# Performance work log

Hardware: AMD Instinct MI355X
Metric: run time of the kernel (lower is better)

## Reference

```python
import jax, jax.numpy as jnp
import numpy as np

B, S, D, DA, DP = 32, 4096, 256, 128, 64


def setup_inputs() -> dict:
    key = jax.random.key(0)
    ks = jax.random.split(key, 10)
    scale = 0.05
    return {
        "h": jax.random.normal(ks[0], (B, S, D), jnp.float32),
        "q": jax.random.normal(ks[1], (B, D), jnp.float32),
        "pf1": jax.random.normal(ks[2], (B, S, DP), jnp.float32),
        "pf2": jax.random.normal(ks[3], (B, S, DP), jnp.float32),
        "Wh": jax.random.normal(ks[4], (DA, D), jnp.float32) * scale,
        "Wq": jax.random.normal(ks[5], (DA, D), jnp.float32) * scale,
        "Wp1": jax.random.normal(ks[6], (DP, DP), jnp.float32) * scale,
        "Wp2": jax.random.normal(ks[7], (DP, DP), jnp.float32) * scale,
        "Wc": jax.random.normal(ks[8], (1, 2 * DA + 2 * DP), jnp.float32) * scale,
        "bc": jax.random.normal(ks[9], (1,), jnp.float32) * scale,
    }


def reference(h, q, pf1, pf2, Wh, Wq, Wp1, Wp2, Wc, bc):
    # h: [B,S,d], q: [B,d], pf1/pf2: [B,S,dp]
    da = Wh.shape[0]
    dp = Wp1.shape[0]
    w = Wc[0]  # [2da+2dp]
    wa, wq, wp1, wp2 = (w[:da], w[da:2 * da], w[2 * da:2 * da + dp], w[2 * da + dp:])
    # context_linear(cat([h_lin, q_lin, pf1_lin, pf2_lin])) decomposes into a sum
    # of per-branch contributions; fuse the two chained matmuls per branch.
    score = (
        h @ (Wh.T @ wa)                 # [B,S]
        + (q @ (Wq.T @ wq))[:, None]    # [B,1] broadcast
        + pf1 @ (Wp1.T @ wp1)           # [B,S]
        + pf2 @ (Wp2.T @ wp2)           # [B,S]
        + bc[0]
    )
    values = jnp.tanh(score)            # dropout is identity in eval
    att = jax.nn.softmax(values, axis=-1)  # [B,S]
    # torch.mean over the stacked S axis -> weighted MEAN, not sum
    context = jnp.einsum('bs,bsd->bd', att, h) / h.shape[1]
    return context
```

## Files before the change

### kernel.cpp

```cpp
#include <hip/hip_runtime.h>
#include <math.h>

#define BB 32
#define SS 4096
#define DD 256
#define DAA 128
#define DPP 64
#define CHUNKS 64
#define ROWS_PER_BLOCK (SS / CHUNKS)
#define WAVES_PER_BLOCK 4
#define ROWS_PER_WAVE (ROWS_PER_BLOCK / WAVES_PER_BLOCK)
#define BATCH 4
#define NBATCH (ROWS_PER_WAVE / BATCH)

#define WS_VH   0
#define WS_VQ   256
#define WS_VP1  512
#define WS_VP2  576
#define WS_BC   640
#define WS_PART 656
#define PART_STRIDE 258

typedef float f4 __attribute__((ext_vector_type(4)));

__global__ void prep_kernel(const float* __restrict__ Wh,
                            const float* __restrict__ Wq,
                            const float* __restrict__ Wp1,
                            const float* __restrict__ Wp2,
                            const float* __restrict__ Wc,
                            const float* __restrict__ bc,
                            float* __restrict__ ws) {
    const int tid = threadIdx.x;
    float vh = 0.f, vq = 0.f;
    for (int a = 0; a < DAA; ++a) {
        vh += Wh[a * DD + tid] * Wc[a];
        vq += Wq[a * DD + tid] * Wc[DAA + a];
    }
    ws[WS_VH + tid] = vh;
    ws[WS_VQ + tid] = vq;
    if (tid < DPP) {
        float vp1 = 0.f, vp2 = 0.f;
        for (int a = 0; a < DPP; ++a) {
            vp1 += Wp1[a * DPP + tid] * Wc[2 * DAA + a];
            vp2 += Wp2[a * DPP + tid] * Wc[2 * DAA + DPP + a];
        }
        ws[WS_VP1 + tid] = vp1;
        ws[WS_VP2 + tid] = vp2;
    }
    if (tid == 0) ws[WS_BC] = bc[0];
}

__global__ __launch_bounds__(256, 8) void
main_kernel(const float* __restrict__ h,
            const float* __restrict__ q,
            const float* __restrict__ pf1,
            const float* __restrict__ pf2,
            float* __restrict__ ws) {
    const int c    = blockIdx.x;
    const int b    = blockIdx.y;
    const int tid  = threadIdx.x;
    const int wave = tid >> 6;
    const int lane = tid & 63;

    const float4 vh4  = ((const float4*)(ws + WS_VH))[lane];
    const float  vp1l = ws[WS_VP1 + lane];
    const float  vp2l = ws[WS_VP2 + lane];

    const float4 q4  = ((const float4*)(q + (size_t)b * DD))[lane];
    const float4 vq4 = ((const float4*)(ws + WS_VQ))[lane];
    float qp = q4.x * vq4.x + q4.y * vq4.y + q4.z * vq4.z + q4.w * vq4.w;
    #pragma unroll
    for (int off = 32; off >= 1; off >>= 1) qp += __shfl_xor(qp, off, 64);
    const float qd = qp + ws[WS_BC];

    const int s0 = c * ROWS_PER_BLOCK + wave * ROWS_PER_WAVE;
    const f4*    hbase  = (const f4*)(h + (size_t)b * SS * DD);
    const float* p1base = pf1 + (size_t)b * SS * DPP;
    const float* p2base = pf2 + (size_t)b * SS * DPP;

    float  l = 0.f;
    float4 ctx = make_float4(0.f, 0.f, 0.f, 0.f);

    for (int ib = 0; ib < NBATCH; ++ib) {
        const int sb = s0 + ib * BATCH;
        f4     h4[BATCH];
        float  p1[BATCH], p2[BATCH], part[BATCH];
        #pragma unroll
        for (int j = 0; j < BATCH; ++j) {
            const int s = sb + j;
            h4[j] = __builtin_nontemporal_load(hbase + (size_t)s * (DD / 4) + lane);
            p1[j] = __builtin_nontemporal_load(p1base + (size_t)s * DPP + lane);
            p2[j] = __builtin_nontemporal_load(p2base + (size_t)s * DPP + lane);
        }
        #pragma unroll
        for (int j = 0; j < BATCH; ++j) {
            part[j] = h4[j].x * vh4.x + h4[j].y * vh4.y
                    + h4[j].z * vh4.z + h4[j].w * vh4.w
                    + p1[j] * vp1l + p2[j] * vp2l;
        }
        #pragma unroll
        for (int off = 32; off >= 1; off >>= 1) {
            #pragma unroll
            for (int j = 0; j < BATCH; ++j)
                part[j] += __shfl_xor(part[j], off, 64);
        }
        #pragma unroll
        for (int j = 0; j < BATCH; ++j) {
            const float score = part[j] + qd;
            const float e2 = __expf(2.f * score);
            const float t  = 1.f - 2.f * __builtin_amdgcn_rcpf(e2 + 1.f);
            const float w  = __expf(t);
            l += w;
            ctx.x += w * h4[j].x;
            ctx.y += w * h4[j].y;
            ctx.z += w * h4[j].z;
            ctx.w += w * h4[j].w;
        }
    }

    __shared__ float s_l[WAVES_PER_BLOCK];
    __shared__ float s_ctx[WAVES_PER_BLOCK][DD];
    if (lane == 0) s_l[wave] = l;
    ((float4*)s_ctx[wave])[lane] = ctx;
    __syncthreads();

    const float cd = s_ctx[0][tid] + s_ctx[1][tid] + s_ctx[2][tid] + s_ctx[3][tid];
    float* part_out = ws + WS_PART + (size_t)(b * CHUNKS + c) * PART_STRIDE;
    part_out[1 + tid] = cd;
    if (tid == 0) part_out[0] = s_l[0] + s_l[1] + s_l[2] + s_l[3];
}

__global__ void finalize_kernel(const float* __restrict__ ws,
                                float* __restrict__ out) {
    const int b   = blockIdx.x;
    const int tid = threadIdx.x;
    __shared__ float s_l[CHUNKS];
    const float* base = ws + WS_PART + (size_t)b * CHUNKS * PART_STRIDE;
    if (tid < CHUNKS) s_l[tid] = base[(size_t)tid * PART_STRIDE];
    __syncthreads();
    float L = 0.f, acc = 0.f;
    #pragma unroll 8
    for (int c = 0; c < CHUNKS; ++c) {
        L   += s_l[c];
        acc += base[(size_t)c * PART_STRIDE + 1 + tid];
    }
    out[b * DD + tid] = acc / (L * (float)SS);
}

extern "C" void kernel_launch(void* const* d_in, const int* in_sizes, int n_in,
                              void* d_out, int out_size, void* d_ws, size_t ws_size,
                              hipStream_t stream) {
    const float* h   = (const float*)d_in[0];
    const float* q   = (const float*)d_in[1];
    const float* pf1 = (const float*)d_in[2];
    const float* pf2 = (const float*)d_in[3];
    const float* Wh  = (const float*)d_in[4];
    const float* Wq  = (const float*)d_in[5];
    const float* Wp1 = (const float*)d_in[6];
    const float* Wp2 = (const float*)d_in[7];
    const float* Wc  = (const float*)d_in[8];
    const float* bc  = (const float*)d_in[9];
    float* out = (float*)d_out;
    float* ws  = (float*)d_ws;

    prep_kernel<<<1, 256, 0, stream>>>(Wh, Wq, Wp1, Wp2, Wc, bc, ws);
    main_kernel<<<dim3(CHUNKS, BB), 256, 0, stream>>>(h, q, pf1, pf2, ws);
    finalize_kernel<<<BB, 256, 0, stream>>>(ws, out);
}
```

Before: 250.3 us.

## Fuse finalize into main kernel via last-block atomic counter, merge pf loads

The separate finalize kernel is removed: each main block bumps a per-batch atomic counter, and the last block to finish reduces the chunk partials and writes the output. The pf1/pf2 loads are merged into one float2 load per lane, with the lower half-wave reading pf1 and the upper half reading pf2. The prep kernel now runs on two blocks and also zeroes the counters. This saves one kernel launch and some load instructions, at the cost of threadfences and a serial tail reduction done by one block per batch.

Measured after the change: 598.7 us. 139% more time.

```diff
diff --git a/kernel.cpp b/kernel.cpp
--- a/kernel.cpp
+++ b/kernel.cpp
@@ -15,13 +15,14 @@
 
 #define WS_VH   0
 #define WS_VQ   256
-#define WS_VP1  512
-#define WS_VP2  576
+#define WS_VP   512
 #define WS_BC   640
-#define WS_PART 656
+#define WS_CNT  644
+#define WS_PART 704
 #define PART_STRIDE 258
 
 typedef float f4 __attribute__((ext_vector_type(4)));
+typedef float f2 __attribute__((ext_vector_type(2)));
 
 __global__ void prep_kernel(const float* __restrict__ Wh,
                             const float* __restrict__ Wq,
@@ -31,23 +32,27 @@
                             const float* __restrict__ bc,
                             float* __restrict__ ws) {
     const int tid = threadIdx.x;
-    float vh = 0.f, vq = 0.f;
-    for (int a = 0; a < DAA; ++a) {
-        vh += Wh[a * DD + tid] * Wc[a];
-        vq += Wq[a * DD + tid] * Wc[DAA + a];
+    if (blockIdx.x == 0) {
+        float vh = 0.f, vq = 0.f;
+        for (int a = 0; a < DAA; ++a) {
+            vh += Wh[a * DD + tid] * Wc[a];
+            vq += Wq[a * DD + tid] * Wc[DAA + a];
+        }
+        ws[WS_VH + tid] = vh;
+        ws[WS_VQ + tid] = vq;
+    } else {
+        if (tid < DPP) {
+            float vp1 = 0.f, vp2 = 0.f;
+            for (int a = 0; a < DPP; ++a) {
+                vp1 += Wp1[a * DPP + tid] * Wc[2 * DAA + a];
+                vp2 += Wp2[a * DPP + tid] * Wc[2 * DAA + DPP + a];
+            }
+            ws[WS_VP + tid]       = vp1;
+            ws[WS_VP + DPP + tid] = vp2;
+        }
+        if (tid == 0) ws[WS_BC] = bc[0];
+        if (tid < BB) ((int*)(ws + WS_CNT))[tid] = 0;
     }
-    ws[WS_VH + tid] = vh;
-    ws[WS_VQ + tid] = vq;
-    if (tid < DPP) {
-        float vp1 = 0.f, vp2 = 0.f;
-        for (int a = 0; a < DPP; ++a) {
-            vp1 += Wp1[a * DPP + tid] * Wc[2 * DAA + a];
-            vp2 += Wp2[a * DPP + tid] * Wc[2 * DAA + DPP + a];
-        }
-        ws[WS_VP1 + tid] = vp1;
-        ws[WS_VP2 + tid] = vp2;
-    }
-    if (tid == 0) ws[WS_BC] = bc[0];
 }
 
 __global__ __launch_bounds__(256, 8) void
@@ -55,16 +60,17 @@
             const float* __restrict__ q,
             const float* __restrict__ pf1,
             const float* __restrict__ pf2,
-            float* __restrict__ ws) {
+            float* __restrict__ ws,
+            float* __restrict__ out) {
     const int c    = blockIdx.x;
     const int b    = blockIdx.y;
     const int tid  = threadIdx.x;
     const int wave = tid >> 6;
     const int lane = tid & 63;
+    const int ll   = lane & 31;
 
-    const float4 vh4  = ((const float4*)(ws + WS_VH))[lane];
-    const float  vp1l = ws[WS_VP1 + lane];
-    const float  vp2l = ws[WS_VP2 + lane];
+    const float4 vh4 = ((const float4*)(ws + WS_VH))[lane];
+    const f2     vpl = ((const f2*)(ws + WS_VP))[lane];
 
     const float4 q4  = ((const float4*)(q + (size_t)b * DD))[lane];
     const float4 vq4 = ((const float4*)(ws + WS_VQ))[lane];
@@ -74,29 +80,28 @@
     const float qd = qp + ws[WS_BC];
 
     const int s0 = c * ROWS_PER_BLOCK + wave * ROWS_PER_WAVE;
-    const f4*    hbase  = (const f4*)(h + (size_t)b * SS * DD);
-    const float* p1base = pf1 + (size_t)b * SS * DPP;
-    const float* p2base = pf2 + (size_t)b * SS * DPP;
+    const f4*    hbase = (const f4*)(h + (size_t)b * SS * DD);
+    const float* pfsel = ((lane < 32) ? pf1 : pf2) + (size_t)b * SS * DPP + 2 * ll;
 
     float  l = 0.f;
     float4 ctx = make_float4(0.f, 0.f, 0.f, 0.f);
 
     for (int ib = 0; ib < NBATCH; ++ib) {
         const int sb = s0 + ib * BATCH;
-        f4     h4[BATCH];
-        float  p1[BATCH], p2[BATCH], part[BATCH];
+        f4    h4[BATCH];
+        f2    pv[BATCH];
+        float part[BATCH];
         #pragma unroll
         for (int j = 0; j < BATCH; ++j) {
             const int s = sb + j;
             h4[j] = __builtin_nontemporal_load(hbase + (size_t)s * (DD / 4) + lane);
-            p1[j] = __builtin_nontemporal_load(p1base + (size_t)s * DPP + lane);
-            p2[j] = __builtin_nontemporal_load(p2base + (size_t)s * DPP + lane);
+            pv[j] = __builtin_nontemporal_load((const f2*)(pfsel + (size_t)s * DPP));
         }
         #pragma unroll
         for (int j = 0; j < BATCH; ++j) {
             part[j] = h4[j].x * vh4.x + h4[j].y * vh4.y
                     + h4[j].z * vh4.z + h4[j].w * vh4.w
-                    + p1[j] * vp1l + p2[j] * vp2l;
+                    + pv[j].x * vpl.x + pv[j].y * vpl.y;
         }
         #pragma unroll
         for (int off = 32; off >= 1; off >>= 1) {
@@ -128,21 +133,22 @@
     float* part_out = ws + WS_PART + (size_t)(b * CHUNKS + c) * PART_STRIDE;
     part_out[1 + tid] = cd;
     if (tid == 0) part_out[0] = s_l[0] + s_l[1] + s_l[2] + s_l[3];
-}
 
-__global__ void finalize_kernel(const float* __restrict__ ws,
-                                float* __restrict__ out) {
-    const int b   = blockIdx.x;
-    const int tid = threadIdx.x;
-    __shared__ float s_l[CHUNKS];
+    __threadfence();
+    __syncthreads();
+    __shared__ int s_last;
+    if (tid == 0)
+        s_last = (atomicAdd((int*)(ws + WS_CNT) + b, 1) == CHUNKS - 1);
+    __syncthreads();
+    if (!s_last) return;
+    __threadfence();
+
     const float* base = ws + WS_PART + (size_t)b * CHUNKS * PART_STRIDE;
-    if (tid < CHUNKS) s_l[tid] = base[(size_t)tid * PART_STRIDE];
-    __syncthreads();
     float L = 0.f, acc = 0.f;
     #pragma unroll 8
-    for (int c = 0; c < CHUNKS; ++c) {
-        L   += s_l[c];
-        acc += base[(size_t)c * PART_STRIDE + 1 + tid];
+    for (int cc = 0; cc < CHUNKS; ++cc) {
+        L   += base[(size_t)cc * PART_STRIDE];
+        acc += base[(size_t)cc * PART_STRIDE + 1 + tid];
     }
     out[b * DD + tid] = acc / (L * (float)SS);
 }
@@ -163,7 +169,6 @@
     float* out = (float*)d_out;
     float* ws  = (float*)d_ws;
 
-    prep_kernel<<<1, 256, 0, stream>>>(Wh, Wq, Wp1, Wp2, Wc, bc, ws);
-    main_kernel<<<dim3(CHUNKS, BB), 256, 0, stream>>>(h, q, pf1, pf2, ws);
-    finalize_kernel<<<BB, 256, 0, stream>>>(ws, out);
+    prep_kernel<<<2, 256, 0, stream>>>(Wh, Wq, Wp1, Wp2, Wc, bc, ws);
+    main_kernel<<<dim3(CHUNKS, BB), 256, 0, stream>>>(h, q, pf1, pf2, ws, out);
 }
```
